# Optimization experiments

Measured on AMD Instinct MI355X. Metric: run time of the kernel, lower is better.

Reference implementation:

```python
import jax, jax.numpy as jnp
import numpy as np

HEADS = 8

def _conv1x1(x, W, b):
    # x: [n, Cin, H, W]; W: [Cout, Cin]; b: [Cout]
    return jnp.einsum('nchw,oc->nohw', x, W) + b[None, :, None, None]

def setup_inputs() -> dict:
    key = jax.random.key(0)
    ks = jax.random.split(key, 11)
    n, Cin, H, W = 8, 256, 80, 80
    Ck, Cv = 256, 256
    s_in = 1.0 / np.sqrt(Cin)
    s_v = 1.0 / np.sqrt(Cv)
    return {
        'query_feature': jax.random.normal(ks[0], (n, Cin, H, W), jnp.float32),
        'key_feature': jax.random.normal(ks[1], (n, Cin, H, W), jnp.float32),
        'value_feature': jax.random.normal(ks[2], (n, Cin, H, W), jnp.float32),
        'Wq': jax.random.normal(ks[3], (Ck, Cin), jnp.float32) * s_in,
        'bq': jax.random.normal(ks[4], (Ck,), jnp.float32) * s_in,
        'Wk': jax.random.normal(ks[5], (Ck, Cin), jnp.float32) * s_in,
        'bk': jax.random.normal(ks[6], (Ck,), jnp.float32) * s_in,
        'Wv': jax.random.normal(ks[7], (Cv, Cin), jnp.float32) * s_in,
        'bv': jax.random.normal(ks[8], (Cv,), jnp.float32) * s_in,
        'Wr': jax.random.normal(ks[9], (Cin, Cv), jnp.float32) * s_v,
        'br': jax.random.normal(ks[10], (Cin,), jnp.float32) * s_v,
    }

def reference(query_feature, key_feature, value_feature, Wq, bq, Wk, bk, Wv, bv, Wr, br):
    n, _, qh, qw = query_feature.shape
    kvn, _, kvh, kvw = key_feature.shape
    Ck = Wq.shape[0]
    Cv = Wv.shape[0]
    hk = Ck // HEADS
    hv = Cv // HEADS
    Lq = qh * qw
    Lkv = kvh * kvw
    # 1x1 conv projections, split channels into heads (consecutive channel blocks)
    q = _conv1x1(query_feature, Wq, bq).reshape(n, HEADS, hk, Lq)
    k = _conv1x1(key_feature, Wk, bk).reshape(kvn, HEADS, hk, Lkv)
    v = _conv1x1(value_feature, Wv, bv).reshape(kvn, HEADS, hv, Lkv)
    # softmax: keys over spatial positions, queries over head channels
    k = jax.nn.softmax(k, axis=3)
    q = jax.nn.softmax(q, axis=2)
    # efficient (linear) attention: context = K @ V^T, out = context^T @ Q
    context = jnp.einsum('nhkl,nhvl->nhkv', k, v)          # [n, H, hk, hv]
    attended = jnp.einsum('nhkv,nhkl->nhvl', context, q)   # [n, H, hv, Lq]
    aggregated = attended.reshape(n, Cv, qh, qw)
    return _conv1x1(aggregated, Wr, br) + query_feature
```

## Files before the change

kernel.cpp:

```cpp
#include <hip/hip_runtime.h>
#include <hip/hip_bf16.h>

#define NB 8
#define C 256
#define LL 6400
#define HEADS 8
#define HC 32
#define NH 64
#define SEG 40
#define SL 160
#define ATP 40
#define QPP 264
#define TPP 272

typedef unsigned short u16;
typedef unsigned int u32;
typedef __attribute__((ext_vector_type(8))) short bf16x8;
typedef __attribute__((ext_vector_type(4))) float f32x4;

typedef __attribute__((address_space(1))) const u32 ga_u32;
typedef __attribute__((address_space(3))) u32 ls_u32;

__device__ __forceinline__ void gload_lds16(const u16* g, u16* l) {
  __builtin_amdgcn_global_load_lds((ga_u32*)g, (ls_u32*)l, 16, 0, 0);
}

__device__ __forceinline__ float bf2f(u32 u) { return __uint_as_float(u << 16); }
__device__ __forceinline__ u16 f2bf(float f) {
  __hip_bfloat16 h = __float2bfloat16(f);
  return *(u16*)&h;
}
__device__ __forceinline__ void unpack8(uint4 u, float* f) {
  f[0] = bf2f(u.x & 0xffffu); f[1] = bf2f(u.x >> 16);
  f[2] = bf2f(u.y & 0xffffu); f[3] = bf2f(u.y >> 16);
  f[4] = bf2f(u.z & 0xffffu); f[5] = bf2f(u.z >> 16);
  f[6] = bf2f(u.w & 0xffffu); f[7] = bf2f(u.w >> 16);
}

struct WcvtArgs { const float* W[3]; u16* Wb[3]; };
struct PFArgs { const float* X[3]; const u16* Wb[3]; const float* bias[3]; u16* P[3]; };

__global__ __launch_bounds__(256) void wcvt(WcvtArgs a) {
  const int idx = blockIdx.x * 256 + threadIdx.x;
  const int which = idx >> 14, off = (idx & 16383) * 4;
  float4 v = *(const float4*)&a.W[which][off];
  ushort4 o = {f2bf(v.x), f2bf(v.y), f2bf(v.z), f2bf(v.w)};
  *(ushort4*)&a.Wb[which][off] = o;
}

__global__ __launch_bounds__(256, 2) void proj_fused(PFArgs args) {
  __shared__ __align__(16) u16 pool[128 * TPP];
  u16* const Atb[2] = {pool, pool + 128 * ATP};
  u16* const Bsb[2] = {pool + 2 * 128 * ATP, pool + 2 * 128 * ATP + 256 * 32};
  const int which = blockIdx.y >> 3, n = blockIdx.y & 7;
  const int l0 = blockIdx.x * 128;
  const int t = threadIdx.x;
  const int lane = t & 63, wave = t >> 6;
  const int fr = lane & 15, q = lane >> 4;
  const int wl = (wave >> 1) * 64, wco = (wave & 1) * 128;
  const int s32 = t & 31, rcg = t >> 5;
  const int srow = t >> 2, scol = (t & 3) * 8;
  const float* X = args.X[which] + (size_t)n * C * LL;
  const u16* Wb = args.Wb[which];
  f32x4 acc[4][8] = {};
  float4 xv[4];

#pragma unroll
  for (int j = 0; j < 4; ++j)
    xv[j] = *(const float4*)&X[(size_t)(rcg * 4 + j) * LL + l0 + s32 * 4];
#pragma unroll
  for (int s = 0; s < 4; ++s)
    gload_lds16(&Wb[(size_t)(s * 64 + srow) * C + scol], &Bsb[0][s * 2048 + wave * 512]);
  {
    const float* xf = (const float*)xv;
#pragma unroll
    for (int li = 0; li < 4; ++li) {
      u32 lo = (u32)f2bf(xf[0 * 4 + li]) | ((u32)f2bf(xf[1 * 4 + li]) << 16);
      u32 hi = (u32)f2bf(xf[2 * 4 + li]) | ((u32)f2bf(xf[3 * 4 + li]) << 16);
      u32* dst = (u32*)&Atb[0][(s32 * 4 + li) * ATP + rcg * 4];
      dst[0] = lo; dst[1] = hi;
    }
  }
  __builtin_amdgcn_sched_barrier(0);
#pragma unroll
  for (int j = 0; j < 4; ++j)
    xv[j] = *(const float4*)&X[(size_t)(32 + rcg * 4 + j) * LL + l0 + s32 * 4];
  asm volatile("s_waitcnt vmcnt(4) lgkmcnt(0)" ::: "memory");
  __builtin_amdgcn_s_barrier();
  __builtin_amdgcn_sched_barrier(0);

#pragma unroll
  for (int kt = 0; kt < 8; ++kt) {
    u16* Atc = Atb[kt & 1];
    u16* Bsc = Bsb[kt & 1];
    if (kt < 7) {
      u16* Atn = Atb[(kt & 1) ^ 1];
      u16* Bsn = Bsb[(kt & 1) ^ 1];
#pragma unroll
      for (int s = 0; s < 4; ++s)
        gload_lds16(&Wb[(size_t)(s * 64 + srow) * C + (kt + 1) * 32 + scol],
                    &Bsn[s * 2048 + wave * 512]);
      const float* xf = (const float*)xv;
#pragma unroll
      for (int li = 0; li < 4; ++li) {
        u32 lo = (u32)f2bf(xf[0 * 4 + li]) | ((u32)f2bf(xf[1 * 4 + li]) << 16);
        u32 hi = (u32)f2bf(xf[2 * 4 + li]) | ((u32)f2bf(xf[3 * 4 + li]) << 16);
        u32* dst = (u32*)&Atn[(s32 * 4 + li) * ATP + rcg * 4];
        dst[0] = lo; dst[1] = hi;
      }
      __builtin_amdgcn_sched_barrier(0);
      if (kt < 6) {
#pragma unroll
        for (int j = 0; j < 4; ++j)
          xv[j] = *(const float4*)&X[(size_t)((kt + 2) * 32 + rcg * 4 + j) * LL + l0 + s32 * 4];
      }
    }
    bf16x8 a[4];
#pragma unroll
    for (int i = 0; i < 4; ++i)
      a[i] = *(const bf16x8*)&Atc[(wl + i * 16 + fr) * ATP + q * 8];
#pragma unroll
    for (int j = 0; j < 8; ++j) {
      bf16x8 b = *(const bf16x8*)&Bsc[(wco + j * 16 + fr) * 32 + q * 8];
#pragma unroll
      for (int i = 0; i < 4; ++i)
        acc[i][j] = __builtin_amdgcn_mfma_f32_16x16x32_bf16(a[i], b, acc[i][j], 0, 0, 0);
    }
    if (kt < 6) {
      asm volatile("s_waitcnt vmcnt(4) lgkmcnt(0)" ::: "memory");
      __builtin_amdgcn_s_barrier();
      __builtin_amdgcn_sched_barrier(0);
    } else if (kt == 6) {
      asm volatile("s_waitcnt vmcnt(0) lgkmcnt(0)" ::: "memory");
      __builtin_amdgcn_s_barrier();
      __builtin_amdgcn_sched_barrier(0);
    }
  }

  const float* bias = args.bias[which];
  u16* P = args.P[which] + (size_t)n * LL * C;
  float bb[8];
#pragma unroll
  for (int j = 0; j < 8; ++j) bb[j] = bias[wco + j * 16 + fr];
  __syncthreads();
#pragma unroll
  for (int i = 0; i < 4; ++i)
#pragma unroll
    for (int r = 0; r < 4; ++r) {
      const int lrow = wl + i * 16 + q * 4 + r;
#pragma unroll
      for (int j = 0; j < 8; ++j)
        pool[lrow * TPP + wco + j * 16 + fr] = f2bf(acc[i][j][r] + bb[j]);
    }
  __syncthreads();
  const int rg = t >> 5, ch = t & 31;
#pragma unroll
  for (int s = 0; s < 16; ++s) {
    const int row = rg * 16 + s;
    bf16x8 vrow = *(const bf16x8*)&pool[row * TPP + ch * 8];
    *(bf16x8*)&P[(size_t)(l0 + row) * C + ch * 8] = vrow;
  }
}

__global__ __launch_bounds__(256) void ctx_part(const u16* __restrict__ Kt,
    const u16* __restrict__ Vt, float* __restrict__ pctx, float* __restrict__ psum) {
  __shared__ __align__(16) u16 Ks[16 * 256];
  __shared__ __align__(16) u16 Vs[16 * 256];
  const int seg = blockIdx.x, n = blockIdx.y;
  const int t = threadIdx.x, lane = t & 63, wave = t >> 6;
  const int l0 = seg * SL;
  const u16* KtN = Kt + (size_t)n * LL * C;
  const u16* VtN = Vt + (size_t)n * LL * C;
  const int k4 = (lane & 7) * 4, v8 = lane >> 3;
  float acc[2][4][4] = {};
  float ssum[2][4] = {};
  for (int ls = 0; ls < SL; ls += 16) {
    __syncthreads();
#pragma unroll
    for (int i = 0; i < 2; ++i) {
      const int r = wave * 4 + i * 2;
      gload_lds16(&KtN[(size_t)(l0 + ls + r) * C + lane * 8], &Ks[r * 256]);
      gload_lds16(&VtN[(size_t)(l0 + ls + r) * C + lane * 8], &Vs[r * 256]);
    }
    __syncthreads();
#pragma unroll
    for (int hh = 0; hh < 2; ++hh) {
      const int h = wave * 2 + hh;
#pragma unroll
      for (int l = 0; l < 16; ++l) {
        ushort4 ku = *(const ushort4*)&Ks[l * 256 + h * 32 + k4];
        ushort4 vu = *(const ushort4*)&Vs[l * 256 + h * 32 + v8 * 4];
        float ek[4] = {__expf(bf2f(ku.x)), __expf(bf2f(ku.y)),
                       __expf(bf2f(ku.z)), __expf(bf2f(ku.w))};
        float vf[4] = {bf2f(vu.x), bf2f(vu.y), bf2f(vu.z), bf2f(vu.w)};
#pragma unroll
        for (int i = 0; i < 4; ++i)
#pragma unroll
          for (int j = 0; j < 4; ++j) acc[hh][i][j] = fmaf(ek[i], vf[j], acc[hh][i][j]);
        if (v8 == 0)
#pragma unroll
          for (int i = 0; i < 4; ++i) ssum[hh][i] += ek[i];
      }
    }
  }
#pragma unroll
  for (int hh = 0; hh < 2; ++hh) {
    const int h = wave * 2 + hh;
    const size_t pb = ((size_t)seg * NH + n * 8 + h) * 1024;
#pragma unroll
    for (int i = 0; i < 4; ++i)
#pragma unroll
      for (int j = 0; j < 4; ++j)
        pctx[pb + (size_t)(k4 + i) * 32 + v8 * 4 + j] = acc[hh][i][j];
    if (v8 == 0) {
      const size_t sb = ((size_t)seg * NH + n * 8 + h) * 32;
#pragma unroll
      for (int i = 0; i < 4; ++i) psum[sb + k4 + i] = ssum[hh][i];
    }
  }
}

__global__ __launch_bounds__(256) void ctx_reduce(const float* __restrict__ pctx,
    const float* __restrict__ psum, float* __restrict__ ctx) {
  const int idx = blockIdx.x * 256 + threadIdx.x;
  const int nh = idx >> 10, e = idx & 1023, k = e >> 5;
  float s = 0.f, ss = 0.f;
  for (int g = 0; g < SEG; ++g) {
    s += pctx[(size_t)(g * NH + nh) * 1024 + e];
    ss += psum[(size_t)(g * NH + nh) * 32 + k];
  }
  ctx[idx] = s / ss;
}

__global__ __launch_bounds__(256) void mfuse(const float* __restrict__ Wr,
    const float* __restrict__ ctx, u16* __restrict__ M) {
  const int idx = blockIdx.x * 256 + threadIdx.x;
  const int hk = idx & 255;
  const int o = (idx >> 8) & 255;
  const int n = idx >> 16;
  const int h = hk >> 5, k = hk & 31;
  const float* wr = Wr + (size_t)o * C + h * HC;
  const float* cx = ctx + ((size_t)(n * HEADS + h) * HC + k) * HC;
  float s = 0.f;
#pragma unroll
  for (int v = 0; v < HC; ++v) s = fmaf(wr[v], cx[v], s);
  M[idx] = f2bf(s);
}

__global__ __launch_bounds__(256) void out_fused(const u16* __restrict__ Qt,
    const u16* __restrict__ Mb, const float* __restrict__ br,
    const float* __restrict__ Xq, float* __restrict__ out) {
  __shared__ __align__(16) u16 Qp[64 * QPP];
  __shared__ __align__(16) u16 As[2][128 * 32];
  const int n = blockIdx.y, l0 = blockIdx.x * 64;
  const int t = threadIdx.x, lane = t & 63, wave = t >> 6;
  const int fr = lane & 15, q = lane >> 4;
  const int wcoL = (wave >> 1) * 64, wl = (wave & 1) * 32;
  const int srow = t >> 2, scol = (t & 3) * 8;
  const u16* QtN = Qt + (size_t)n * LL * C;
  const u16* MbN = Mb + (size_t)n * C * C;

#pragma unroll
  for (int s = 0; s < 2; ++s)
    gload_lds16(&MbN[(size_t)(s * 64 + srow) * C + scol], &As[0][s * 2048 + wave * 512]);

#pragma unroll
  for (int p = 0; p < 2; ++p) {
    const int row = p * 32 + (t >> 3);
    const int g = t & 7;
    const uint4* src = (const uint4*)&QtN[(size_t)(l0 + row) * C + g * 32];
    uint4 u0 = src[0], u1 = src[1], u2 = src[2], u3 = src[3];
    float v[32];
    unpack8(u0, v); unpack8(u1, v + 8); unpack8(u2, v + 16); unpack8(u3, v + 24);
    float e[32], s = 0.f;
#pragma unroll
    for (int j = 0; j < 32; ++j) { e[j] = __expf(v[j]); s += e[j]; }
    const float r = 1.0f / s;
    uint4* drow = (uint4*)&Qp[row * QPP + g * 32];
#pragma unroll
    for (int b4 = 0; b4 < 4; ++b4) {
      union { uint4 u; u16 h[8]; } o;
#pragma unroll
      for (int j = 0; j < 8; ++j) o.h[j] = f2bf(e[b4 * 8 + j] * r);
      drow[b4] = o.u;
    }
  }
  asm volatile("s_waitcnt vmcnt(0) lgkmcnt(0)" ::: "memory");
  __builtin_amdgcn_s_barrier();
  __builtin_amdgcn_sched_barrier(0);

  f32x4 acc[2][4][2] = {};
#pragma unroll
  for (int it = 0; it < 16; ++it) {
    const int coh = it >> 3, k0 = (it & 7) * 32, cur = it & 1;
    if (it < 15) {
      const int nco = (it + 1) >> 3, nk0 = ((it + 1) & 7) * 32;
#pragma unroll
      for (int s = 0; s < 2; ++s)
        gload_lds16(&MbN[(size_t)(nco * 128 + s * 64 + srow) * C + nk0 + scol],
                    &As[cur ^ 1][s * 2048 + wave * 512]);
      __builtin_amdgcn_sched_barrier(0);
    }
    bf16x8 a[4], b[2];
#pragma unroll
    for (int i = 0; i < 4; ++i)
      a[i] = *(const bf16x8*)&As[cur][(wcoL + i * 16 + fr) * 32 + q * 8];
#pragma unroll
    for (int j = 0; j < 2; ++j)
      b[j] = *(const bf16x8*)&Qp[(wl + j * 16 + fr) * QPP + k0 + q * 8];
#pragma unroll
    for (int i = 0; i < 4; ++i)
#pragma unroll
      for (int j = 0; j < 2; ++j)
        acc[coh][i][j] = __builtin_amdgcn_mfma_f32_16x16x32_bf16(a[i], b[j], acc[coh][i][j], 0, 0, 0);
    if (it < 15) {
      asm volatile("s_waitcnt vmcnt(0) lgkmcnt(0)" ::: "memory");
      __builtin_amdgcn_s_barrier();
      __builtin_amdgcn_sched_barrier(0);
    }
  }

  const float* XqN = Xq + (size_t)n * C * LL;
  float* On = out + (size_t)n * C * LL;
#pragma unroll
  for (int coh = 0; coh < 2; ++coh)
#pragma unroll
    for (int i = 0; i < 4; ++i)
#pragma unroll
      for (int r = 0; r < 4; ++r) {
        const int co = coh * 128 + wcoL + i * 16 + q * 4 + r;
        const float bb = br[co];
#pragma unroll
        for (int j = 0; j < 2; ++j) {
          const int l = l0 + wl + j * 16 + fr;
          const size_t off = (size_t)co * LL + l;
          On[off] = acc[coh][i][j][r] + bb + XqN[off];
        }
      }
}

extern "C" void kernel_launch(void* const* d_in, const int* in_sizes, int n_in,
                              void* d_out, int out_size, void* d_ws, size_t ws_size,
                              hipStream_t stream) {
  const float* Xq = (const float*)d_in[0];
  const float* Xk = (const float*)d_in[1];
  const float* Xv = (const float*)d_in[2];
  const float* Wq = (const float*)d_in[3];
  const float* bq = (const float*)d_in[4];
  const float* Wk = (const float*)d_in[5];
  const float* bk = (const float*)d_in[6];
  const float* Wv = (const float*)d_in[7];
  const float* bv = (const float*)d_in[8];
  const float* Wr = (const float*)d_in[9];
  const float* br = (const float*)d_in[10];
  float* out = (float*)d_out;

  char* ws = (char*)d_ws;
  const size_t nelem = (size_t)NB * LL * C;
  u16* Qt = (u16*)ws;
  u16* Kt = (u16*)(ws + nelem * 2);
  u16* Vt = (u16*)(ws + nelem * 4);
  char* p = ws + nelem * 6;
  u16* Wqb = (u16*)p; p += C * C * 2;
  u16* Wkb = (u16*)p; p += C * C * 2;
  u16* Wvb = (u16*)p; p += C * C * 2;
  float* pctx = (float*)p; p += (size_t)SEG * NH * HC * HC * 4;
  float* psum = (float*)p; p += (size_t)SEG * NH * HC * 4;
  float* ctx = (float*)p;  p += (size_t)NH * HC * HC * 4;
  u16* Mb = (u16*)p;

  WcvtArgs wa;
  wa.W[0] = Wq; wa.W[1] = Wk; wa.W[2] = Wv;
  wa.Wb[0] = Wqb; wa.Wb[1] = Wkb; wa.Wb[2] = Wvb;
  wcvt<<<192, 256, 0, stream>>>(wa);

  PFArgs pa;
  pa.X[0] = Xq; pa.X[1] = Xk; pa.X[2] = Xv;
  pa.Wb[0] = Wqb; pa.Wb[1] = Wkb; pa.Wb[2] = Wvb;
  pa.bias[0] = bq; pa.bias[1] = bk; pa.bias[2] = bv;
  pa.P[0] = Qt; pa.P[1] = Kt; pa.P[2] = Vt;
  proj_fused<<<dim3(50, 24), 256, 0, stream>>>(pa);

  ctx_part<<<dim3(SEG, NB), 256, 0, stream>>>(Kt, Vt, pctx, psum);
  ctx_reduce<<<NH * HC * HC / 256, 256, 0, stream>>>(pctx, psum, ctx);
  mfuse<<<NB * C * C / 256, 256, 0, stream>>>(Wr, ctx, Mb);
  out_fused<<<dim3(100, NB), 256, 0, stream>>>(Qt, Mb, br, Xq, out);
}
```

Before: 321.2 us.

## Halve projection GEMM tile to 64 rows and raise occupancy to three blocks

```diff
diff --git a/kernel.cpp b/kernel.cpp
--- a/kernel.cpp
+++ b/kernel.cpp
@@ -48,93 +48,74 @@
   *(ushort4*)&a.Wb[which][off] = o;
 }
 
-__global__ __launch_bounds__(256, 2) void proj_fused(PFArgs args) {
-  __shared__ __align__(16) u16 pool[128 * TPP];
-  u16* const Atb[2] = {pool, pool + 128 * ATP};
-  u16* const Bsb[2] = {pool + 2 * 128 * ATP, pool + 2 * 128 * ATP + 256 * 32};
+__global__ __launch_bounds__(256, 3) void proj_fused(PFArgs args) {
+  __shared__ __align__(16) u16 pool[2 * 64 * ATP + 2 * 256 * 32];
+  u16* const Atb[2] = {pool, pool + 64 * ATP};
+  u16* const Bsb[2] = {pool + 2 * 64 * ATP, pool + 2 * 64 * ATP + 256 * 32};
   const int which = blockIdx.y >> 3, n = blockIdx.y & 7;
-  const int l0 = blockIdx.x * 128;
+  const int l0 = blockIdx.x * 64;
   const int t = threadIdx.x;
   const int lane = t & 63, wave = t >> 6;
   const int fr = lane & 15, q = lane >> 4;
-  const int wl = (wave >> 1) * 64, wco = (wave & 1) * 128;
-  const int s32 = t & 31, rcg = t >> 5;
+  const int wl = (wave & 1) * 32, wco = (wave >> 1) * 128;
+  const int s16 = t & 15, rc2 = t >> 4;
   const int srow = t >> 2, scol = (t & 3) * 8;
   const float* X = args.X[which] + (size_t)n * C * LL;
   const u16* Wb = args.Wb[which];
-  f32x4 acc[4][8] = {};
-  float4 xv[4];
-
-#pragma unroll
-  for (int j = 0; j < 4; ++j)
-    xv[j] = *(const float4*)&X[(size_t)(rcg * 4 + j) * LL + l0 + s32 * 4];
+  f32x4 acc[2][8] = {};
+  float4 xv[2];
+
+  xv[0] = *(const float4*)&X[(size_t)(rc2 * 2 + 0) * LL + l0 + s16 * 4];
+  xv[1] = *(const float4*)&X[(size_t)(rc2 * 2 + 1) * LL + l0 + s16 * 4];
 #pragma unroll
   for (int s = 0; s < 4; ++s)
     gload_lds16(&Wb[(size_t)(s * 64 + srow) * C + scol], &Bsb[0][s * 2048 + wave * 512]);
   {
-    const float* xf = (const float*)xv;
-#pragma unroll
-    for (int li = 0; li < 4; ++li) {
-      u32 lo = (u32)f2bf(xf[0 * 4 + li]) | ((u32)f2bf(xf[1 * 4 + li]) << 16);
-      u32 hi = (u32)f2bf(xf[2 * 4 + li]) | ((u32)f2bf(xf[3 * 4 + li]) << 16);
-      u32* dst = (u32*)&Atb[0][(s32 * 4 + li) * ATP + rcg * 4];
-      dst[0] = lo; dst[1] = hi;
-    }
-  }
-  __builtin_amdgcn_sched_barrier(0);
-#pragma unroll
-  for (int j = 0; j < 4; ++j)
-    xv[j] = *(const float4*)&X[(size_t)(32 + rcg * 4 + j) * LL + l0 + s32 * 4];
-  asm volatile("s_waitcnt vmcnt(4) lgkmcnt(0)" ::: "memory");
-  __builtin_amdgcn_s_barrier();
-  __builtin_amdgcn_sched_barrier(0);
+    const float* x0 = (const float*)&xv[0];
+    const float* x1 = (const float*)&xv[1];
+#pragma unroll
+    for (int j = 0; j < 4; ++j) {
+      u32 pk = (u32)f2bf(x0[j]) | ((u32)f2bf(x1[j]) << 16);
+      *(u32*)&Atb[0][(s16 * 4 + j) * ATP + rc2 * 2] = pk;
+    }
+  }
+  __syncthreads();
 
 #pragma unroll
   for (int kt = 0; kt < 8; ++kt) {
     u16* Atc = Atb[kt & 1];
     u16* Bsc = Bsb[kt & 1];
     if (kt < 7) {
-      u16* Atn = Atb[(kt & 1) ^ 1];
-      u16* Bsn = Bsb[(kt & 1) ^ 1];
+      xv[0] = *(const float4*)&X[(size_t)((kt + 1) * 32 + rc2 * 2 + 0) * LL + l0 + s16 * 4];
+      xv[1] = *(const float4*)&X[(size_t)((kt + 1) * 32 + rc2 * 2 + 1) * LL + l0 + s16 * 4];
+      u16* Bsn = Bsb[(kt + 1) & 1];
 #pragma unroll
       for (int s = 0; s < 4; ++s)
         gload_lds16(&Wb[(size_t)(s * 64 + srow) * C + (kt + 1) * 32 + scol],
                     &Bsn[s * 2048 + wave * 512]);
-      const float* xf = (const float*)xv;
-#pragma unroll
-      for (int li = 0; li < 4; ++li) {
-        u32 lo = (u32)f2bf(xf[0 * 4 + li]) | ((u32)f2bf(xf[1 * 4 + li]) << 16);
-        u32 hi = (u32)f2bf(xf[2 * 4 + li]) | ((u32)f2bf(xf[3 * 4 + li]) << 16);
-        u32* dst = (u32*)&Atn[(s32 * 4 + li) * ATP + rcg * 4];
-        dst[0] = lo; dst[1] = hi;
-      }
-      __builtin_amdgcn_sched_barrier(0);
-      if (kt < 6) {
-#pragma unroll
-        for (int j = 0; j < 4; ++j)
-          xv[j] = *(const float4*)&X[(size_t)((kt + 2) * 32 + rcg * 4 + j) * LL + l0 + s32 * 4];
-      }
-    }
-    bf16x8 a[4];
-#pragma unroll
-    for (int i = 0; i < 4; ++i)
+    }
+    bf16x8 a[2];
+#pragma unroll
+    for (int i = 0; i < 2; ++i)
       a[i] = *(const bf16x8*)&Atc[(wl + i * 16 + fr) * ATP + q * 8];
 #pragma unroll
     for (int j = 0; j < 8; ++j) {
       bf16x8 b = *(const bf16x8*)&Bsc[(wco + j * 16 + fr) * 32 + q * 8];
 #pragma unroll
-      for (int i = 0; i < 4; ++i)
+      for (int i = 0; i < 2; ++i)
         acc[i][j] = __builtin_amdgcn_mfma_f32_16x16x32_bf16(a[i], b, acc[i][j], 0, 0, 0);
     }
-    if (kt < 6) {
-      asm volatile("s_waitcnt vmcnt(4) lgkmcnt(0)" ::: "memory");
-      __builtin_amdgcn_s_barrier();
-      __builtin_amdgcn_sched_barrier(0);
-    } else if (kt == 6) {
-      asm volatile("s_waitcnt vmcnt(0) lgkmcnt(0)" ::: "memory");
-      __builtin_amdgcn_s_barrier();
-      __builtin_amdgcn_sched_barrier(0);
-    }
+    if (kt < 7) {
+      u16* Atn = Atb[(kt + 1) & 1];
+      const float* x0 = (const float*)&xv[0];
+      const float* x1 = (const float*)&xv[1];
+#pragma unroll
+      for (int j = 0; j < 4; ++j) {
+        u32 pk = (u32)f2bf(x0[j]) | ((u32)f2bf(x1[j]) << 16);
+        *(u32*)&Atn[(s16 * 4 + j) * ATP + rc2 * 2] = pk;
+      }
+    }
+    __syncthreads();
   }
 
   const float* bias = args.bias[which];
@@ -142,9 +123,8 @@
   float bb[8];
 #pragma unroll
   for (int j = 0; j < 8; ++j) bb[j] = bias[wco + j * 16 + fr];
-  __syncthreads();
-#pragma unroll
-  for (int i = 0; i < 4; ++i)
+#pragma unroll
+  for (int i = 0; i < 2; ++i)
 #pragma unroll
     for (int r = 0; r < 4; ++r) {
       const int lrow = wl + i * 16 + q * 4 + r;
@@ -155,8 +135,8 @@
   __syncthreads();
   const int rg = t >> 5, ch = t & 31;
 #pragma unroll
-  for (int s = 0; s < 16; ++s) {
-    const int row = rg * 16 + s;
+  for (int s = 0; s < 8; ++s) {
+    const int row = rg * 8 + s;
     bf16x8 vrow = *(const bf16x8*)&pool[row * TPP + ch * 8];
     *(bf16x8*)&P[(size_t)(l0 + row) * C + ch * 8] = vrow;
   }
@@ -379,7 +359,7 @@
   pa.Wb[0] = Wqb; pa.Wb[1] = Wkb; pa.Wb[2] = Wvb;
   pa.bias[0] = bq; pa.bias[1] = bk; pa.bias[2] = bv;
   pa.P[0] = Qt; pa.P[1] = Kt; pa.P[2] = Vt;
-  proj_fused<<<dim3(50, 24), 256, 0, stream>>>(pa);
+  proj_fused<<<dim3(100, 24), 256, 0, stream>>>(pa);
 
   ctx_part<<<dim3(SEG, NB), 256, 0, stream>>>(Kt, Vt, pctx, psum);
   ctx_reduce<<<NH * HC * HC / 256, 256, 0, stream>>>(pctx, psum, ctx);
```

Measured after the change: 327.9 us. 1.02x slower.
